# Kernel tuning notes

Hardware: AMD Instinct MI355X
Metric: run time of the kernel (lower is better)

Reference implementation:

```python
import jax, jax.numpy as jnp
import numpy as np

NUM_Q, NUM_P = 64, 1024


def setup_inputs() -> dict:
    key = jax.random.key(0)
    k1, k2 = jax.random.split(key)
    pred = jax.random.normal(k1, (NUM_Q, NUM_P), dtype=jnp.float32)
    y = (jax.random.uniform(k2, (NUM_Q, NUM_P)) < 0.1).astype(jnp.float32)
    return {"pred": pred, "y": y}


def reference(pred, y):
    # Original: for each query i, for each relevant index j (y[i,j]==1),
    # MarginRankingLoss(sum)(x1=pred[i,j].repeat(P), x2=pred[i], target=(y[i]!=1))
    # with margin=0: per-element loss = max(0, -t*(x1-x2)).
    #   t=0 (relevant k):     max(0, 0) = 0
    #   t=1 (non-relevant k): max(0, pred[i,k] - pred[i,j])
    # => loss[i] = sum_{j: rel} sum_{k: non-rel} relu(pred[i,k] - pred[i,j])
    # result = loss.mean() over queries. (bce branch disabled in config.)
    rel = (y == 1.0)                       # [Q,P] relevant mask (j axis)
    neg = ~rel                             # [Q,P] non-relevant mask (k axis)
    # diff[i,j,k] = pred[i,k] - pred[i,j]
    diff = pred[:, None, :] - pred[:, :, None]          # [Q,P,P]
    pair_mask = rel[:, :, None] & neg[:, None, :]       # [Q,P,P]
    hinge = jnp.where(pair_mask, jnp.maximum(diff, 0.0), 0.0)
    loss = jnp.sum(hinge, axis=(1, 2))                  # [Q]
    return jnp.mean(loss)
```

## Files before the change

### kernel.cpp

```cpp
#include <hip/hip_runtime.h>
#include <math.h>

#define NUM_Q 64
#define NUM_P 1024
#define BLOCK 256
#define SPLIT 4
#define NPAD  1028

__global__ __launch_bounds__(BLOCK) void per_query_loss_kernel(
    const float* __restrict__ pred,
    const float* __restrict__ y,
    float* __restrict__ out)
{
    __shared__ __align__(16) float relVals[NPAD];
    __shared__ int   relCount;
    __shared__ float waveSums[BLOCK / 64];

    const int q    = blockIdx.x >> 2;
    const int s    = blockIdx.x & 3;
    const int tid  = threadIdx.x;
    const int wave = tid >> 6;
    const int lane = tid & 63;

    if (tid == 0) atomicCAS((unsigned int*)out, 0xAAAAAAAAu, 0u);

    const float4* __restrict__ prow4 = (const float4*)(pred + q * NUM_P);
    const float4* __restrict__ yrow4 = (const float4*)(y    + q * NUM_P);

    const float4 p4 = prow4[tid];
    const float4 y4 = yrow4[tid];

    for (int i = tid; i < NPAD; i += BLOCK) relVals[i] = INFINITY;
    if (tid == 0) relCount = 0;
    __syncthreads();

    const bool r0 = (y4.x == 1.0f), r1 = (y4.y == 1.0f);
    const bool r2 = (y4.z == 1.0f), r3 = (y4.w == 1.0f);
    const unsigned long long m0 = __ballot(r0);
    const unsigned long long m1 = __ballot(r1);
    const unsigned long long m2 = __ballot(r2);
    const unsigned long long m3 = __ballot(r3);
    const int c0 = __popcll(m0), c1 = __popcll(m1);
    const int c2 = __popcll(m2), c3 = __popcll(m3);
    const int total = c0 + c1 + c2 + c3;
    int base = 0;
    if (lane == 0 && total) base = atomicAdd(&relCount, total);
    base = __shfl(base, 0, 64);
    const unsigned long long lt = (1ull << lane) - 1ull;
    if (r0) relVals[base                + __popcll(m0 & lt)] = p4.x;
    if (r1) relVals[base + c0           + __popcll(m1 & lt)] = p4.y;
    if (r2) relVals[base + c0 + c1      + __popcll(m2 & lt)] = p4.z;
    if (r3) relVals[base + c0 + c1 + c2 + __popcll(m3 & lt)] = p4.w;

    float pe, ye;
    if      (s == 0) { pe = p4.x; ye = y4.x; }
    else if (s == 1) { pe = p4.y; ye = y4.y; }
    else if (s == 2) { pe = p4.z; ye = y4.z; }
    else             { pe = p4.w; ye = y4.w; }
    const float mp = (ye == 1.0f) ? -INFINITY : pe;
    __syncthreads();

    const int nChunks = (relCount + 3) >> 2;
    const float4* __restrict__ rv4 = (const float4*)relVals;

    float a0 = 0.0f, a1 = 0.0f, a2 = 0.0f, a3 = 0.0f;
    #pragma unroll 2
    for (int c = 0; c < nChunks; ++c) {
        const float4 rv = rv4[c];
        a0 += fmaxf(mp - rv.x, 0.0f);
        a1 += fmaxf(mp - rv.y, 0.0f);
        a2 += fmaxf(mp - rv.z, 0.0f);
        a3 += fmaxf(mp - rv.w, 0.0f);
    }
    float acc = (a0 + a1) + (a2 + a3);

    #pragma unroll
    for (int off = 32; off > 0; off >>= 1)
        acc += __shfl_down(acc, off, 64);
    if (lane == 0) waveSums[wave] = acc;
    __syncthreads();

    if (wave == 0) {
        float v = (lane < BLOCK / 64) ? waveSums[lane] : 0.0f;
        v += __shfl_down(v, 2, 64);
        v += __shfl_down(v, 1, 64);
        if (lane == 0)
            atomicAdd(out, v * (1.0f / NUM_Q));
    }
}

extern "C" void kernel_launch(void* const* d_in, const int* in_sizes, int n_in,
                              void* d_out, int out_size, void* d_ws, size_t ws_size,
                              hipStream_t stream) {
    const float* pred = (const float*)d_in[0];
    const float* y    = (const float*)d_in[1];
    float* out = (float*)d_out;

    per_query_loss_kernel<<<NUM_Q * SPLIT, BLOCK, 0, stream>>>(pred, y, out);
}
```

Before: 60.45 us.

## Process all four elements per thread with per-wave relevant lists, one block per query

Replaces the 4-way split of each query across blocks with a single block per query, where each thread handles all four of its elements against the relevant values. Relevant values are compacted into per-wave shared regions padded with INFINITY, which removes the shared-memory atomic and the initialisation pass plus its barrier. Each LDS read of relevant values is now reused across four non-relevant candidates, raising arithmetic per load. The cost is only 64 blocks, fewer than the GPU's compute units, so parallelism and latency hiding drop.

```diff
diff --git a/kernel.cpp b/kernel.cpp
--- a/kernel.cpp
+++ b/kernel.cpp
@@ -4,35 +4,27 @@
 #define NUM_Q 64
 #define NUM_P 1024
 #define BLOCK 256
-#define SPLIT 4
-#define NPAD  1028
+#define WAVES (BLOCK / 64)
+#define REG   260
 
 __global__ __launch_bounds__(BLOCK) void per_query_loss_kernel(
     const float* __restrict__ pred,
     const float* __restrict__ y,
     float* __restrict__ out)
 {
-    __shared__ __align__(16) float relVals[NPAD];
-    __shared__ int   relCount;
-    __shared__ float waveSums[BLOCK / 64];
+    __shared__ __align__(16) float relVals[WAVES][REG];
+    __shared__ int   nChunks[WAVES];
+    __shared__ float waveSums[WAVES];
 
-    const int q    = blockIdx.x >> 2;
-    const int s    = blockIdx.x & 3;
+    const int q    = blockIdx.x;
     const int tid  = threadIdx.x;
     const int wave = tid >> 6;
     const int lane = tid & 63;
 
     if (tid == 0) atomicCAS((unsigned int*)out, 0xAAAAAAAAu, 0u);
 
-    const float4* __restrict__ prow4 = (const float4*)(pred + q * NUM_P);
-    const float4* __restrict__ yrow4 = (const float4*)(y    + q * NUM_P);
-
-    const float4 p4 = prow4[tid];
-    const float4 y4 = yrow4[tid];
-
-    for (int i = tid; i < NPAD; i += BLOCK) relVals[i] = INFINITY;
-    if (tid == 0) relCount = 0;
-    __syncthreads();
+    const float4 p4 = ((const float4*)(pred + q * NUM_P))[tid];
+    const float4 y4 = ((const float4*)(y    + q * NUM_P))[tid];
 
     const bool r0 = (y4.x == 1.0f), r1 = (y4.y == 1.0f);
     const bool r2 = (y4.z == 1.0f), r3 = (y4.w == 1.0f);
@@ -42,35 +34,38 @@
     const unsigned long long m3 = __ballot(r3);
     const int c0 = __popcll(m0), c1 = __popcll(m1);
     const int c2 = __popcll(m2), c3 = __popcll(m3);
-    const int total = c0 + c1 + c2 + c3;
-    int base = 0;
-    if (lane == 0 && total) base = atomicAdd(&relCount, total);
-    base = __shfl(base, 0, 64);
+    const int cw = c0 + c1 + c2 + c3;
     const unsigned long long lt = (1ull << lane) - 1ull;
-    if (r0) relVals[base                + __popcll(m0 & lt)] = p4.x;
-    if (r1) relVals[base + c0           + __popcll(m1 & lt)] = p4.y;
-    if (r2) relVals[base + c0 + c1      + __popcll(m2 & lt)] = p4.z;
-    if (r3) relVals[base + c0 + c1 + c2 + __popcll(m3 & lt)] = p4.w;
+    float* __restrict__ reg = relVals[wave];
+    if (r0) reg[               __popcll(m0 & lt)] = p4.x;
+    if (r1) reg[c0           + __popcll(m1 & lt)] = p4.y;
+    if (r2) reg[c0 + c1      + __popcll(m2 & lt)] = p4.z;
+    if (r3) reg[c0 + c1 + c2 + __popcll(m3 & lt)] = p4.w;
+    if (lane < 4) reg[cw + lane] = INFINITY;
+    if (lane == 0) nChunks[wave] = (cw + 3) >> 2;
 
-    float pe, ye;
-    if      (s == 0) { pe = p4.x; ye = y4.x; }
-    else if (s == 1) { pe = p4.y; ye = y4.y; }
-    else if (s == 2) { pe = p4.z; ye = y4.z; }
-    else             { pe = p4.w; ye = y4.w; }
-    const float mp = (ye == 1.0f) ? -INFINITY : pe;
+    const float mp0 = r0 ? -INFINITY : p4.x;
+    const float mp1 = r1 ? -INFINITY : p4.y;
+    const float mp2 = r2 ? -INFINITY : p4.z;
+    const float mp3 = r3 ? -INFINITY : p4.w;
     __syncthreads();
 
-    const int nChunks = (relCount + 3) >> 2;
-    const float4* __restrict__ rv4 = (const float4*)relVals;
-
     float a0 = 0.0f, a1 = 0.0f, a2 = 0.0f, a3 = 0.0f;
-    #pragma unroll 2
-    for (int c = 0; c < nChunks; ++c) {
-        const float4 rv = rv4[c];
-        a0 += fmaxf(mp - rv.x, 0.0f);
-        a1 += fmaxf(mp - rv.y, 0.0f);
-        a2 += fmaxf(mp - rv.z, 0.0f);
-        a3 += fmaxf(mp - rv.w, 0.0f);
+    for (int w = 0; w < WAVES; ++w) {
+        const float4* __restrict__ rv4 = (const float4*)relVals[w];
+        const int nc = nChunks[w];
+        #pragma unroll 2
+        for (int c = 0; c < nc; ++c) {
+            const float4 rv = rv4[c];
+            a0 += fmaxf(mp0 - rv.x, 0.0f) + fmaxf(mp0 - rv.y, 0.0f)
+                + fmaxf(mp0 - rv.z, 0.0f) + fmaxf(mp0 - rv.w, 0.0f);
+            a1 += fmaxf(mp1 - rv.x, 0.0f) + fmaxf(mp1 - rv.y, 0.0f)
+                + fmaxf(mp1 - rv.z, 0.0f) + fmaxf(mp1 - rv.w, 0.0f);
+            a2 += fmaxf(mp2 - rv.x, 0.0f) + fmaxf(mp2 - rv.y, 0.0f)
+                + fmaxf(mp2 - rv.z, 0.0f) + fmaxf(mp2 - rv.w, 0.0f);
+            a3 += fmaxf(mp3 - rv.x, 0.0f) + fmaxf(mp3 - rv.y, 0.0f)
+                + fmaxf(mp3 - rv.z, 0.0f) + fmaxf(mp3 - rv.w, 0.0f);
+        }
     }
     float acc = (a0 + a1) + (a2 + a3);
 
@@ -81,7 +76,7 @@
     __syncthreads();
 
     if (wave == 0) {
-        float v = (lane < BLOCK / 64) ? waveSums[lane] : 0.0f;
+        float v = (lane < WAVES) ? waveSums[lane] : 0.0f;
         v += __shfl_down(v, 2, 64);
         v += __shfl_down(v, 1, 64);
         if (lane == 0)
@@ -96,5 +91,5 @@
     const float* y    = (const float*)d_in[1];
     float* out = (float*)d_out;
 
-    per_query_loss_kernel<<<NUM_Q * SPLIT, BLOCK, 0, stream>>>(pred, y, out);
+    per_query_loss_kernel<<<NUM_Q, BLOCK, 0, stream>>>(pred, y, out);
 }
```

Result: faster. 59.12 us (-2.2%).
